# Kernel optimization log

Hardware: AMD Instinct MI355X
Metric: run time of the kernel (lower is better)

## Reference

```python
import jax, jax.numpy as jnp
import numpy as np

VOCAB = 100000
EMB = 256
HID = 512
H = HID // 2            # per-direction hidden size
T_LEN = 2048
N_TAGS = 7
START, END = 5, 6
NEG = -10000.0


def setup_inputs() -> dict:
    key = jax.random.key(0)
    ks = jax.random.split(key, 16)
    n = lambda k, sh: jax.random.normal(k, sh, dtype=jnp.float32)
    bound = 1.0 / np.sqrt(H)  # torch LSTM/Linear-style init scale
    u = lambda k, sh: jax.random.uniform(k, sh, dtype=jnp.float32, minval=-bound, maxval=bound)
    transitions = n(ks[12], (N_TAGS, N_TAGS))
    transitions = transitions.at[:, START].set(NEG).at[END, :].set(NEG)
    return {
        "words": jax.random.randint(ks[0], (T_LEN,), 0, VOCAB),
        "embed": n(ks[1], (VOCAB + 1, EMB)),
        "W_ih_f": u(ks[2], (4 * H, EMB)),
        "W_hh_f": u(ks[3], (4 * H, H)),
        "b_ih_f": u(ks[4], (4 * H,)),
        "b_hh_f": u(ks[5], (4 * H,)),
        "W_ih_b": u(ks[6], (4 * H, EMB)),
        "W_hh_b": u(ks[7], (4 * H, H)),
        "b_ih_b": u(ks[8], (4 * H,)),
        "b_hh_b": u(ks[9], (4 * H,)),
        "W_out": u(ks[10], (N_TAGS, HID)),
        "b_out": u(ks[11], (N_TAGS,)),
        "transitions": transitions,
        "h0": n(ks[13], (2, H)),
        "c0": n(ks[14], (2, H)),
    }


def _lstm_dir(xs, h0, c0, Wih, Whh, bih, bhh):
    # xs: [T, EMB]; torch gate order i, f, g, o
    def step(carry, x):
        h, c = carry
        g = x @ Wih.T + bih + h @ Whh.T + bhh  # [4H]
        i, f, gg, o = jnp.split(g, 4)
        i, f, o = jax.nn.sigmoid(i), jax.nn.sigmoid(f), jax.nn.sigmoid(o)
        c = f * c + i * jnp.tanh(gg)
        h = o * jnp.tanh(c)
        return (h, c), h
    _, hs = jax.lax.scan(step, (h0, c0), xs)
    return hs  # [T, H]


def _features(words, embed, W_ih_f, W_hh_f, b_ih_f, b_hh_f,
              W_ih_b, W_hh_b, b_ih_b, b_hh_b, W_out, b_out, h0, c0):
    xs = embed[words]                                   # [T, EMB]
    hs_f = _lstm_dir(xs, h0[0], c0[0], W_ih_f, W_hh_f, b_ih_f, b_hh_f)
    hs_b = _lstm_dir(xs[::-1], h0[1], c0[1], W_ih_b, W_hh_b, b_ih_b, b_hh_b)[::-1]
    lstm_out = jnp.concatenate([hs_f, hs_b], axis=1)    # [T, HID]
    return lstm_out @ W_out.T + b_out                   # [T, N_TAGS]


def _viterbi(feats, transitions):
    init = jnp.full((N_TAGS,), NEG, dtype=feats.dtype).at[START].set(0.0)

    def vit_step(fv, feat):
        # torch code: next_tag_var[j] = forward_var + transitions[j]
        M = fv[None, :] + transitions          # [j, i] = fv[i] + T[j, i]
        bp = jnp.argmax(M, axis=1)             # [N_TAGS] best prev tag
        fv_new = jnp.max(M, axis=1) + feat
        return fv_new, bp

    fv, bptrs = jax.lax.scan(vit_step, init, feats)     # bptrs: [T, N_TAGS]
    terminal = fv + transitions[END]
    final_tag = jnp.argmax(terminal)
    path_score = terminal[final_tag]

    def back_step(tag, bp):
        return bp[tag], tag
    _start, path = jax.lax.scan(back_step, final_tag, bptrs, reverse=True)
    return path_score, path  # path: [T] tag ids (B/I/E/S/N = 0..4)


def reference(words, embed, W_ih_f, W_hh_f, b_ih_f, b_hh_f,
              W_ih_b, W_hh_b, b_ih_b, b_hh_b, W_out, b_out,
              transitions, h0, c0):
    feats = _features(words, embed, W_ih_f, W_hh_f, b_ih_f, b_hh_f,
                      W_ih_b, W_hh_b, b_ih_b, b_hh_b, W_out, b_out, h0, c0)
    return _viterbi(feats, transitions)
```

## Files before the change

### kernel.cpp

```cpp
#include <hip/hip_runtime.h>

typedef unsigned int u32;

#define T_LEN 2048
#define NEG (-10000.0f)
#define WSCALE 2032.0f
#define HSCALE 127.0f
#define SCALE_INV (1.0f / (2032.0f * 127.0f))

#define DOT(acc, w, hs) \
  asm("v_dot4_i32_i8 %0, %2, %1, %0" : "+v"(acc) : "v"(w), "s"(hs))

__device__ __forceinline__ u32 rdlane_u32(u32 v, int lane) {
#if __has_builtin(__builtin_amdgcn_readlane)
  return (u32)__builtin_amdgcn_readlane((int)v, lane);
#else
  return (u32)__shfl((int)v, lane);
#endif
}

__device__ __forceinline__ float rdlane_f32(float v, int lane) {
  return __builtin_bit_cast(float, rdlane_u32(__builtin_bit_cast(u32, v), lane));
}

__device__ __forceinline__ void block_sync_lds() {
  asm volatile("s_waitcnt lgkmcnt(0)" ::: "memory");
  __builtin_amdgcn_s_barrier();
}

__global__ void pack_whh_i8(const float* __restrict__ Wf,
                            const float* __restrict__ Wb,
                            u32* __restrict__ WP) {
  int idx = blockIdx.x * 256 + threadIdx.x;
  int d   = idx >> 16;
  int rem = idx & 65535;
  int q   = rem >> 12;
  int r   = (rem >> 2) & 1023;
  int j   = rem & 3;
  const float* W = d ? Wb : Wf;
  float4 v = *(const float4*)&W[r * 256 + q * 16 + j * 4];
  int b0 = (int)rintf(fminf(fmaxf(v.x * WSCALE, -127.f), 127.f));
  int b1 = (int)rintf(fminf(fmaxf(v.y * WSCALE, -127.f), 127.f));
  int b2 = (int)rintf(fminf(fmaxf(v.z * WSCALE, -127.f), 127.f));
  int b3 = (int)rintf(fminf(fmaxf(v.w * WSCALE, -127.f), 127.f));
  WP[((d * 16 + q) * 1024 + r) * 4 + j] =
      (u32)(b0 & 255) | ((u32)(b1 & 255) << 8) |
      ((u32)(b2 & 255) << 16) | ((u32)(b3 & 255) << 24);
}

__global__ void gather_kernel(const int* __restrict__ words,
                              const float* __restrict__ embed,
                              float* __restrict__ xs) {
  int t = blockIdx.x;
  int k = threadIdx.x;
  xs[t * 256 + k] = embed[(size_t)words[t] * 256 + k];
}

__global__ __launch_bounds__(256) void gemm_xw(
    const float* __restrict__ xs,
    const float* __restrict__ Wf, const float* __restrict__ Wb,
    const float* __restrict__ bihf, const float* __restrict__ bhhf,
    const float* __restrict__ bihb, const float* __restrict__ bhhb,
    float* __restrict__ XW) {
  __shared__ float lx[32 * 256];
  __shared__ float lw[32 * 132];
  const int tid = threadIdx.x;
  const int t0 = blockIdx.x * 32;
  const int g0 = blockIdx.y * 128;
  const int d  = blockIdx.z;
  const float* W = d ? Wb : Wf;

  #pragma unroll 4
  for (int r = 0; r < 32; ++r) lx[r * 256 + tid] = xs[(t0 + r) * 256 + tid];

  const int tg = tid & 31, tt = tid >> 5;
  float acc[4][4] = {};

  for (int kc = 0; kc < 8; ++kc) {
    __syncthreads();
    #pragma unroll
    for (int r2 = 0; r2 < 16; ++r2) {
      int gg = r2 * 8 + (tid >> 5);
      int k  = tid & 31;
      lw[k * 132 + gg] = W[(g0 + gg) * 256 + kc * 32 + k];
    }
    __syncthreads();
    #pragma unroll
    for (int k = 0; k < 32; ++k) {
      float4 wv = *(const float4*)&lw[k * 132 + tg * 4];
      #pragma unroll
      for (int a = 0; a < 4; ++a) {
        float xa = lx[(tt * 4 + a) * 256 + kc * 32 + k];
        acc[a][0] = fmaf(xa, wv.x, acc[a][0]);
        acc[a][1] = fmaf(xa, wv.y, acc[a][1]);
        acc[a][2] = fmaf(xa, wv.z, acc[a][2]);
        acc[a][3] = fmaf(xa, wv.w, acc[a][3]);
      }
    }
  }
  const float* bih = d ? bihb : bihf;
  const float* bhh = d ? bhhb : bhhf;
  int gcol = g0 + tg * 4;
  float4 bb;
  bb.x = bih[gcol + 0] + bhh[gcol + 0];
  bb.y = bih[gcol + 1] + bhh[gcol + 1];
  bb.z = bih[gcol + 2] + bhh[gcol + 2];
  bb.w = bih[gcol + 3] + bhh[gcol + 3];
  #pragma unroll
  for (int a = 0; a < 4; ++a) {
    float4 o;
    o.x = acc[a][0] + bb.x;
    o.y = acc[a][1] + bb.y;
    o.z = acc[a][2] + bb.z;
    o.w = acc[a][3] + bb.w;
    *(float4*)&XW[((size_t)d * T_LEN + t0 + tt * 4 + a) * 1024 + gcol] = o;
  }
}

__global__ void __launch_bounds__(512)
__attribute__((amdgpu_waves_per_eu(2, 2)))
lstm_seq(
    const float* __restrict__ XW, float* __restrict__ HS,
    const u32* __restrict__ wpack,
    const float* __restrict__ h0, const float* __restrict__ c0) {
  __shared__ u32   H8[64];
  __shared__ float GT[1024];
  const int tid = threadIdx.x;
  const int d = blockIdx.x;
  const int lane = tid & 63;

  uint4 w0[16], w1[16];
  const uint4* wr = (const uint4*)wpack;
  #pragma unroll
  for (int q = 0; q < 16; ++q) {
    w0[q] = wr[(d * 16 + q) * 1024 + tid];
    w1[q] = wr[(d * 16 + q) * 1024 + tid + 512];
  }

  float c = 0.0f, h = 0.0f;
  if (tid < 256) {
    c = c0[d * 256 + tid];
    h = h0[d * 256 + tid];
    int hi = (int)rintf(fminf(fmaxf(h, -1.0f), 1.0f) * HSCALE);
    ((unsigned char*)H8)[tid] = (unsigned char)(hi & 255);
  }
  block_sync_lds();
  u32 hA = H8[lane];

  const int delta = d ? -1024 : 1024;
  const float* xwp = XW + ((size_t)d * T_LEN + (d ? (T_LEN - 1) : 0)) * 1024 + tid;
  float xw0c = xwp[0], xw1c = xwp[512];

  for (int s = 0; s < T_LEN; ++s) {
    float xw0n = 0.0f, xw1n = 0.0f;
    if (s < T_LEN - 1) { xwp += delta; xw0n = xwp[0]; xw1n = xwp[512]; }

    int a0 = 0, b0 = 0;
    int a1 = 0, b1 = 0;
    {
      u32 s0 = rdlane_u32(hA, 0);
      u32 s1 = rdlane_u32(hA, 1);
      u32 s2 = rdlane_u32(hA, 2);
      u32 s3 = rdlane_u32(hA, 3);
      #pragma unroll
      for (int q = 0; q < 16; ++q) {
        u32 n0 = 0, n1 = 0, n2 = 0, n3 = 0;
        if (q < 15) {
          n0 = rdlane_u32(hA, 4 * q + 4);
          n1 = rdlane_u32(hA, 4 * q + 5);
          n2 = rdlane_u32(hA, 4 * q + 6);
          n3 = rdlane_u32(hA, 4 * q + 7);
        }
        DOT(a0, w0[q].x, s0);
        DOT(a1, w1[q].x, s0);
        DOT(b0, w0[q].y, s1);
        DOT(b1, w1[q].y, s1);
        DOT(a0, w0[q].z, s2);
        DOT(a1, w1[q].z, s2);
        DOT(b0, w0[q].w, s3);
        DOT(b1, w1[q].w, s3);
        s0 = n0; s1 = n1; s2 = n2; s3 = n3;
      }
    }
    GT[tid]       = fmaf((float)(a0 + b0), SCALE_INV, xw0c);
    GT[tid + 512] = fmaf((float)(a1 + b1), SCALE_INV, xw1c);
    block_sync_lds();

    const int t = d ? (T_LEN - 1 - s) : s;
    if (tid < 256) {
      float gi = GT[tid];
      float gf = GT[256 + tid];
      float gc = GT[512 + tid];
      float go = GT[768 + tid];
      gi = 1.0f / (1.0f + __expf(-gi));
      gf = 1.0f / (1.0f + __expf(-gf));
      go = 1.0f / (1.0f + __expf(-go));
      gc = 1.0f - 2.0f / (__expf(2.0f * gc) + 1.0f);
      c = gf * c + gi * gc;
      float th = 1.0f - 2.0f / (__expf(2.0f * c) + 1.0f);
      h = go * th;
      HS[((size_t)d * T_LEN + t) * 256 + tid] = h;
      int hi = (int)rintf(h * HSCALE);
      ((unsigned char*)H8)[tid] = (unsigned char)(hi & 255);
    }
    block_sync_lds();
    hA = H8[lane];
    xw0c = xw0n;
    xw1c = xw1n;
  }
}

__global__ void feats_kernel(const float* __restrict__ hs,
                             const float* __restrict__ wout,
                             const float* __restrict__ bout,
                             float* __restrict__ feats) {
  __shared__ float lf[16 * 257];
  __shared__ float lb[16 * 257];
  const int tid = threadIdx.x;
  const int t0 = blockIdx.x * 16;
  for (int i = tid; i < 16 * 256; i += 128) {
    int r = i >> 8, k = i & 255;
    lf[r * 257 + k] = hs[(size_t)(t0 + r) * 256 + k];
    lb[r * 257 + k] = hs[(size_t)T_LEN * 256 + (size_t)(t0 + r) * 256 + k];
  }
  __syncthreads();
  const int tl = tid >> 3, n = tid & 7;
  if (n < 7) {
    float acc = bout[n];
    #pragma unroll 8
    for (int k = 0; k < 256; ++k) acc = fmaf(lf[tl * 257 + k], wout[n * 512 + k], acc);
    #pragma unroll 8
    for (int k = 0; k < 256; ++k) acc = fmaf(lb[tl * 257 + k], wout[n * 512 + 256 + k], acc);
    feats[(t0 + tl) * 7 + n] = acc;
  }
}

__global__ __launch_bounds__(256) void viterbi_kernel(
    const float* __restrict__ feats,
    const float* __restrict__ trans,
    float* __restrict__ out) {
  extern __shared__ char vsm[];
  float*         fe = (float*)vsm;
  unsigned char* bp = (unsigned char*)(vsm + 57344);
  unsigned char* G  = (unsigned char*)(vsm + 73728);
  unsigned char* bt = (unsigned char*)(vsm + 73984);
  const int tid = threadIdx.x;

  for (int i = tid; i < T_LEN * 7; i += 256) fe[i] = feats[i];
  __syncthreads();

  if (tid < 64) {
    const int j  = tid;
    const int jc = (j < 7) ? j : 0;
    float Trow[7];
    #pragma unroll
    for (int i = 0; i < 7; ++i) Trow[i] = trans[jc * 7 + i];
    float fv = (j == 5) ? 0.0f : NEG;
    for (int t = 0; t < T_LEN; ++t) {
      float f0 = rdlane_f32(fv, 0), f1 = rdlane_f32(fv, 1), f2 = rdlane_f32(fv, 2),
            f3 = rdlane_f32(fv, 3), f4 = rdlane_f32(fv, 4), f5 = rdlane_f32(fv, 5),
            f6 = rdlane_f32(fv, 6);
      float v0 = f0 + Trow[0], v1 = f1 + Trow[1], v2 = f2 + Trow[2],
            v3 = f3 + Trow[3], v4 = f4 + Trow[4], v5 = f5 + Trow[5],
            v6 = f6 + Trow[6];
      bool c01 = v0 >= v1;  float m01 = c01 ? v0 : v1;  int i01 = c01 ? 0 : 1;
      bool c23 = v2 >= v3;  float m23 = c23 ? v2 : v3;  int i23 = c23 ? 2 : 3;
      bool c45 = v4 >= v5;  float m45 = c45 ? v4 : v5;  int i45 = c45 ? 4 : 5;
      bool cA  = m01 >= m23; float mA = cA ? m01 : m23; int iA = cA ? i01 : i23;
      bool cB  = m45 >= v6;  float mB = cB ? m45 : v6;  int iB = cB ? i45 : 6;
      bool cF  = mA >= mB;   float best = cF ? mA : mB; int bi = cF ? iA : iB;
      if (j < 7) bp[t * 8 + j] = (unsigned char)bi;
      fv = best + fe[t * 7 + jc];
    }
    float term = fv + trans[42 + jc];
    float best = rdlane_f32(term, 0); int btag = 0;
    #pragma unroll
    for (int i = 1; i < 7; ++i) {
      float ti = rdlane_f32(term, i);
      if (ti > best) { best = ti; btag = i; }
    }
    if (j == 0) {
      out[0] = best;
      bt[31] = (unsigned char)btag;
    }
  }
  __syncthreads();

  {
    const int s = tid >> 3, j = tid & 7;
    if (s < 32 && j < 7) {
      int g = j;
      for (int t = s * 64 + 63; t >= s * 64; --t) g = bp[t * 8 + g];
      G[s * 8 + j] = (unsigned char)g;
    }
  }
  __syncthreads();

  if (tid == 0) {
    int x = bt[31];
    for (int s = 31; s >= 1; --s) { x = G[s * 8 + x]; bt[s - 1] = (unsigned char)x; }
  }
  __syncthreads();

  if (tid < 32) {
    const int s = tid;
    int tag = bt[s];
    for (int t = s * 64 + 63; t >= s * 64; --t) {
      out[1 + t] = (float)tag;
      tag = bp[t * 8 + tag];
    }
  }
}

extern "C" void kernel_launch(void* const* d_in, const int* in_sizes, int n_in,
                              void* d_out, int out_size, void* d_ws, size_t ws_size,
                              hipStream_t stream) {
  const int*   words = (const int*)d_in[0];
  const float* embed = (const float*)d_in[1];
  const float* Wih_f = (const float*)d_in[2];
  const float* Whh_f = (const float*)d_in[3];
  const float* bih_f = (const float*)d_in[4];
  const float* bhh_f = (const float*)d_in[5];
  const float* Wih_b = (const float*)d_in[6];
  const float* Whh_b = (const float*)d_in[7];
  const float* bih_b = (const float*)d_in[8];
  const float* bhh_b = (const float*)d_in[9];
  const float* Wout  = (const float*)d_in[10];
  const float* bout  = (const float*)d_in[11];
  const float* trans = (const float*)d_in[12];
  const float* h0    = (const float*)d_in[13];
  const float* c0    = (const float*)d_in[14];

  float* ws = (float*)d_ws;
  float* XW = ws;
  float* HS = ws + 4194304;
  float* XS = ws + 5242880;
  float* FE = ws + 5767168;
  u32*   WP = (u32*)(ws + 5781504);

  pack_whh_i8<<<512, 256, 0, stream>>>(Whh_f, Whh_b, WP);
  gather_kernel<<<T_LEN, 256, 0, stream>>>(words, embed, XS);
  dim3 ggrid(T_LEN / 32, 1024 / 128, 2);
  gemm_xw<<<ggrid, 256, 0, stream>>>(XS, Wih_f, Wih_b, bih_f, bhh_f, bih_b, bhh_b, XW);
  lstm_seq<<<2, 512, 0, stream>>>(XW, HS, WP, h0, c0);
  feats_kernel<<<128, 128, 0, stream>>>(HS, Wout, bout, FE);
  viterbi_kernel<<<1, 256, 74048, stream>>>(FE, trans, (float*)d_out);
}
```

Before: 2.569 ms.

## Give each LSTM thread one hidden unit with all four gate weights in registers

The recurrent kernel now launches 256 threads per direction instead of 512. Each thread keeps the int8 weights for all four gates of its hidden unit in registers, and the weight pack layout is reordered to match. The gate activations are computed in-thread, so the LDS gate staging and one of the two barriers per timestep go away, and the h buffer is double-buffered. In exchange each thread performs twice as many dot4 instructions per step with half as many waves, and register pressure rises sharply.

Result: no change. 2.549 ms (-0.8%).

```diff
diff --git a/kernel.cpp b/kernel.cpp
--- a/kernel.cpp
+++ b/kernel.cpp
@@ -8,8 +8,18 @@
 #define HSCALE 127.0f
 #define SCALE_INV (1.0f / (2032.0f * 127.0f))
 
-#define DOT(acc, w, hs) \
-  asm("v_dot4_i32_i8 %0, %2, %1, %0" : "+v"(acc) : "v"(w), "s"(hs))
+__device__ __forceinline__ int sdot4(u32 a, u32 b, int c) {
+#if __has_builtin(__builtin_amdgcn_sdot4)
+  return __builtin_amdgcn_sdot4((int)a, (int)b, c, false);
+#else
+  int r = c;
+  r += (int)(signed char)(a)       * (int)(signed char)(b);
+  r += (int)(signed char)(a >> 8)  * (int)(signed char)(b >> 8);
+  r += (int)(signed char)(a >> 16) * (int)(signed char)(b >> 16);
+  r += (int)(signed char)(a >> 24) * (int)(signed char)(b >> 24);
+  return r;
+#endif
+}
 
 __device__ __forceinline__ u32 rdlane_u32(u32 v, int lane) {
 #if __has_builtin(__builtin_amdgcn_readlane)
@@ -33,17 +43,17 @@
                             u32* __restrict__ WP) {
   int idx = blockIdx.x * 256 + threadIdx.x;
   int d   = idx >> 16;
-  int rem = idx & 65535;
-  int q   = rem >> 12;
-  int r   = (rem >> 2) & 1023;
-  int j   = rem & 3;
+  int G   = (idx >> 14) & 3;
+  int q4  = (idx >> 10) & 15;
+  int c   = (idx >> 2) & 255;
+  int j   = idx & 3;
   const float* W = d ? Wb : Wf;
-  float4 v = *(const float4*)&W[r * 256 + q * 16 + j * 4];
+  float4 v = *(const float4*)&W[(G * 256 + c) * 256 + q4 * 16 + j * 4];
   int b0 = (int)rintf(fminf(fmaxf(v.x * WSCALE, -127.f), 127.f));
   int b1 = (int)rintf(fminf(fmaxf(v.y * WSCALE, -127.f), 127.f));
   int b2 = (int)rintf(fminf(fmaxf(v.z * WSCALE, -127.f), 127.f));
   int b3 = (int)rintf(fminf(fmaxf(v.w * WSCALE, -127.f), 127.f));
-  WP[((d * 16 + q) * 1024 + r) * 4 + j] =
+  WP[(((d * 4 + G) * 16 + q4) * 256 + c) * 4 + j] =
       (u32)(b0 & 255) | ((u32)(b1 & 255) << 8) |
       ((u32)(b2 & 255) << 16) | ((u32)(b3 & 255) << 24);
 }
@@ -117,96 +127,89 @@
   }
 }
 
-__global__ void __launch_bounds__(512)
-__attribute__((amdgpu_waves_per_eu(2, 2)))
+__global__ void __launch_bounds__(256)
+__attribute__((amdgpu_waves_per_eu(1, 1)))
 lstm_seq(
     const float* __restrict__ XW, float* __restrict__ HS,
     const u32* __restrict__ wpack,
     const float* __restrict__ h0, const float* __restrict__ c0) {
-  __shared__ u32   H8[64];
-  __shared__ float GT[1024];
+  __shared__ u32 H8[2][64];
   const int tid = threadIdx.x;
   const int d = blockIdx.x;
   const int lane = tid & 63;
 
-  uint4 w0[16], w1[16];
-  const uint4* wr = (const uint4*)wpack;
-  #pragma unroll
-  for (int q = 0; q < 16; ++q) {
-    w0[q] = wr[(d * 16 + q) * 1024 + tid];
-    w1[q] = wr[(d * 16 + q) * 1024 + tid + 512];
-  }
-
-  float c = 0.0f, h = 0.0f;
-  if (tid < 256) {
-    c = c0[d * 256 + tid];
-    h = h0[d * 256 + tid];
+  u32 wIv[64], wFv[64], wGv[64], wOv[64];
+  {
+    const uint4* wr = (const uint4*)wpack;
+    #pragma unroll
+    for (int q4 = 0; q4 < 16; ++q4) {
+      uint4 t;
+      t = wr[((d * 4 + 0) * 16 + q4) * 256 + tid];
+      wIv[q4 * 4 + 0] = t.x; wIv[q4 * 4 + 1] = t.y;
+      wIv[q4 * 4 + 2] = t.z; wIv[q4 * 4 + 3] = t.w;
+      t = wr[((d * 4 + 1) * 16 + q4) * 256 + tid];
+      wFv[q4 * 4 + 0] = t.x; wFv[q4 * 4 + 1] = t.y;
+      wFv[q4 * 4 + 2] = t.z; wFv[q4 * 4 + 3] = t.w;
+      t = wr[((d * 4 + 2) * 16 + q4) * 256 + tid];
+      wGv[q4 * 4 + 0] = t.x; wGv[q4 * 4 + 1] = t.y;
+      wGv[q4 * 4 + 2] = t.z; wGv[q4 * 4 + 3] = t.w;
+      t = wr[((d * 4 + 3) * 16 + q4) * 256 + tid];
+      wOv[q4 * 4 + 0] = t.x; wOv[q4 * 4 + 1] = t.y;
+      wOv[q4 * 4 + 2] = t.z; wOv[q4 * 4 + 3] = t.w;
+    }
+  }
+
+  float c = c0[d * 256 + tid];
+  float h = h0[d * 256 + tid];
+  {
     int hi = (int)rintf(fminf(fmaxf(h, -1.0f), 1.0f) * HSCALE);
-    ((unsigned char*)H8)[tid] = (unsigned char)(hi & 255);
+    ((unsigned char*)&H8[0][0])[tid] = (unsigned char)(hi & 255);
   }
   block_sync_lds();
-  u32 hA = H8[lane];
+  u32 hA = H8[0][lane];
 
   const int delta = d ? -1024 : 1024;
   const float* xwp = XW + ((size_t)d * T_LEN + (d ? (T_LEN - 1) : 0)) * 1024 + tid;
-  float xw0c = xwp[0], xw1c = xwp[512];
+  float xi = xwp[0], xf = xwp[256], xg = xwp[512], xo = xwp[768];
 
   for (int s = 0; s < T_LEN; ++s) {
-    float xw0n = 0.0f, xw1n = 0.0f;
-    if (s < T_LEN - 1) { xwp += delta; xw0n = xwp[0]; xw1n = xwp[512]; }
-
-    int a0 = 0, b0 = 0;
-    int a1 = 0, b1 = 0;
-    {
-      u32 s0 = rdlane_u32(hA, 0);
-      u32 s1 = rdlane_u32(hA, 1);
-      u32 s2 = rdlane_u32(hA, 2);
-      u32 s3 = rdlane_u32(hA, 3);
-      #pragma unroll
-      for (int q = 0; q < 16; ++q) {
-        u32 n0 = 0, n1 = 0, n2 = 0, n3 = 0;
-        if (q < 15) {
-          n0 = rdlane_u32(hA, 4 * q + 4);
-          n1 = rdlane_u32(hA, 4 * q + 5);
-          n2 = rdlane_u32(hA, 4 * q + 6);
-          n3 = rdlane_u32(hA, 4 * q + 7);
-        }
-        DOT(a0, w0[q].x, s0);
-        DOT(a1, w1[q].x, s0);
-        DOT(b0, w0[q].y, s1);
-        DOT(b1, w1[q].y, s1);
-        DOT(a0, w0[q].z, s2);
-        DOT(a1, w1[q].z, s2);
-        DOT(b0, w0[q].w, s3);
-        DOT(b1, w1[q].w, s3);
-        s0 = n0; s1 = n1; s2 = n2; s3 = n3;
-      }
-    }
-    GT[tid]       = fmaf((float)(a0 + b0), SCALE_INV, xw0c);
-    GT[tid + 512] = fmaf((float)(a1 + b1), SCALE_INV, xw1c);
+    float ni = 0.f, nf = 0.f, ng = 0.f, no = 0.f;
+    if (s < T_LEN - 1) {
+      xwp += delta;
+      ni = xwp[0]; nf = xwp[256]; ng = xwp[512]; no = xwp[768];
+    }
+
+    int aI = 0, aF = 0, aG = 0, aO = 0;
+    #pragma unroll
+    for (int q = 0; q < 64; ++q) {
+      u32 sv = rdlane_u32(hA, q);
+      aI = sdot4(wIv[q], sv, aI);
+      aF = sdot4(wFv[q], sv, aF);
+      aG = sdot4(wGv[q], sv, aG);
+      aO = sdot4(wOv[q], sv, aO);
+    }
+
+    float gi = fmaf((float)aI, SCALE_INV, xi);
+    float gf = fmaf((float)aF, SCALE_INV, xf);
+    float gc = fmaf((float)aG, SCALE_INV, xg);
+    float go = fmaf((float)aO, SCALE_INV, xo);
+    gi = 1.0f / (1.0f + __expf(-gi));
+    gf = 1.0f / (1.0f + __expf(-gf));
+    go = 1.0f / (1.0f + __expf(-go));
+    gc = 1.0f - 2.0f / (__expf(2.0f * gc) + 1.0f);
+    c = gf * c + gi * gc;
+    float th = 1.0f - 2.0f / (__expf(2.0f * c) + 1.0f);
+    h = go * th;
+
+    const int t = d ? (T_LEN - 1 - s) : s;
+    HS[((size_t)d * T_LEN + t) * 256 + tid] = h;
+
+    int hi = (int)rintf(h * HSCALE);
+    const int wbuf = (s + 1) & 1;
+    ((unsigned char*)&H8[wbuf][0])[tid] = (unsigned char)(hi & 255);
     block_sync_lds();
-
-    const int t = d ? (T_LEN - 1 - s) : s;
-    if (tid < 256) {
-      float gi = GT[tid];
-      float gf = GT[256 + tid];
-      float gc = GT[512 + tid];
-      float go = GT[768 + tid];
-      gi = 1.0f / (1.0f + __expf(-gi));
-      gf = 1.0f / (1.0f + __expf(-gf));
-      go = 1.0f / (1.0f + __expf(-go));
-      gc = 1.0f - 2.0f / (__expf(2.0f * gc) + 1.0f);
-      c = gf * c + gi * gc;
-      float th = 1.0f - 2.0f / (__expf(2.0f * c) + 1.0f);
-      h = go * th;
-      HS[((size_t)d * T_LEN + t) * 256 + tid] = h;
-      int hi = (int)rintf(h * HSCALE);
-      ((unsigned char*)H8)[tid] = (unsigned char)(hi & 255);
-    }
-    block_sync_lds();
-    hA = H8[lane];
-    xw0c = xw0n;
-    xw1c = xw1n;
+    hA = H8[wbuf][lane];
+    xi = ni; xf = nf; xg = ng; xo = no;
   }
 }
 
@@ -342,7 +345,7 @@
   gather_kernel<<<T_LEN, 256, 0, stream>>>(words, embed, XS);
   dim3 ggrid(T_LEN / 32, 1024 / 128, 2);
   gemm_xw<<<ggrid, 256, 0, stream>>>(XS, Wih_f, Wih_b, bih_f, bhh_f, bih_b, bhh_b, XW);
-  lstm_seq<<<2, 512, 0, stream>>>(XW, HS, WP, h0, c0);
+  lstm_seq<<<2, 256, 0, stream>>>(XW, HS, WP, h0, c0);
   feats_kernel<<<128, 128, 0, stream>>>(HS, Wout, bout, FE);
   viterbi_kernel<<<1, 256, 74048, stream>>>(FE, trans, (float*)d_out);
 }
```
